# Kernel optimization log

Hardware: AMD Instinct MI355X
Metric: run time of the kernel (lower is better)

## Reference

```python
import jax, jax.numpy as jnp
import numpy as np

N_NODES = 50000
N_EDGES = 800000
IN_FT = 128
HID_FT = 64
EMB_FT = 128
NUM_LAYERS = 4
NEG_SLOP = 0.2


def setup_inputs() -> dict:
    key = jax.random.key(0)
    ks = jax.random.split(key, 16)
    x = jax.random.normal(ks[0], (N_NODES, IN_FT), dtype=jnp.float32)
    edge_index = jax.random.randint(ks[1], (2, N_EDGES), 0, N_NODES, dtype=jnp.int64)
    edge_weight = jax.random.uniform(ks[2], (N_EDGES,), dtype=jnp.float32)
    def lin(k, fin, fout):
        s = 1.0 / np.sqrt(fin)
        kw, kb = jax.random.split(k)
        W = jax.random.uniform(kw, (fin, fout), minval=-s, maxval=s, dtype=jnp.float32)
        b = jax.random.uniform(kb, (fout,), minval=-s, maxval=s, dtype=jnp.float32)
        return W, b
    W1, b1 = lin(ks[3], IN_FT, HID_FT)
    W2, b2 = lin(ks[4], HID_FT, HID_FT)
    W3, b3 = lin(ks[5], HID_FT, HID_FT)
    W4, b4 = lin(ks[6], HID_FT, HID_FT)
    Wh, bh = lin(ks[7], NUM_LAYERS * HID_FT, EMB_FT)
    return {"x": x, "edge_index": edge_index, "edge_weight": edge_weight,
            "W1": W1, "b1": b1, "W2": W2, "b2": b2, "W3": W3, "b3": b3,
            "W4": W4, "b4": b4, "Wh": Wh, "bh": bh}


def _gcn_no_norm(x, src, dst, ew, W, b):
    # GCNConv(add_self_loops=False, normalize=False): plain weighted scatter-add
    h = x @ W                                   # [N, F]
    msg = h[src] * ew[:, None]                  # gather over edges [E, F]
    return jax.ops.segment_sum(msg, dst, num_segments=N_NODES) + b


def _gcn_norm(x, src, dst, ew, W, b):
    # Default GCNConv: add self loops (weight 1) + symmetric normalization.
    deg = jax.ops.segment_sum(ew, dst, num_segments=N_NODES) + 1.0  # +1 self loop
    dinv = jnp.where(deg > 0, jax.lax.rsqrt(deg), 0.0)
    norm = dinv[src] * ew * dinv[dst]           # [E]
    h = x @ W
    agg = jax.ops.segment_sum(h[src] * norm[:, None], dst, num_segments=N_NODES)
    agg = agg + (dinv * dinv)[:, None] * h      # self-loop term
    return agg + b


def _forward(x, edge_index, edge_weight, W1, b1, W2, b2, W3, b3, W4, b4, Wh, bh):
    src, dst = edge_index[0], edge_index[1]
    lrelu = lambda v: jax.nn.leaky_relu(v, NEG_SLOP)
    outs = []
    h = lrelu(_gcn_no_norm(x, src, dst, edge_weight, W1, b1))
    outs.append(h)  # dropout is identity in deterministic reference
    for W, b in ((W2, b2), (W3, b3), (W4, b4)):
        h = lrelu(_gcn_norm(h, src, dst, edge_weight, W, b))
        outs.append(h)
    cat = jnp.concatenate(outs, axis=-1)        # [N, num_layers*HID_FT]
    return cat @ Wh + bh


def reference(x, edge_index, edge_weight, W1, b1, W2, b2, W3, b3, W4, b4, Wh, bh):
    return _forward(x, edge_index, edge_weight, W1, b1, W2, b2, W3, b3, W4, b4, Wh, bh)
```

## Files before the change

### kernel.cpp

```cpp
#include <hip/hip_runtime.h>
#include <hip/hip_bf16.h>

#define NEG_SLOP 0.2f
typedef unsigned long long ull;
typedef __attribute__((ext_vector_type(8))) short bf16x8;
typedef __attribute__((ext_vector_type(4))) float f32x4;

__device__ __forceinline__ float lrelu(float v) { return v > 0.0f ? v : NEG_SLOP * v; }

__device__ __forceinline__ float bf2f(unsigned short u) {
    union { unsigned int i; float f; } c; c.i = ((unsigned int)u) << 16; return c.f;
}
__device__ __forceinline__ unsigned short f2bf(float f) {
    union { float f; unsigned int i; } c; c.f = f;
    unsigned int r = c.i + 0x7FFF + ((c.i >> 16) & 1);
    return (unsigned short)(r >> 16);
}

__global__ void prep_kernel(const float* __restrict__ Wh, unsigned short* __restrict__ wht,
                            float4* __restrict__ pz, int nz) {
    int idx = blockIdx.x * 256 + threadIdx.x;
    if (idx < nz) pz[idx] = make_float4(0.f, 0.f, 0.f, 0.f);
    if (idx < 256 * 128) {
        int k = idx >> 7, c = idx & 127;
        wht[(size_t)c * 256 + k] = f2bf(Wh[idx]);
    }
}

__global__ void histo_kernel(const int* __restrict__ dst, const float* __restrict__ ew,
                             ull* __restrict__ packed4, int* __restrict__ rank,
                             int n_edges, int n) {
    int e = blockIdx.x * 256 + threadIdx.x;
    if (e >= n_edges) return;
    int d = dst[e];
    int c = e & 3;
    ull delta = (1ULL << 40) | (ull)(ew[e] * 4294967296.0f);
    ull old = atomicAdd(&packed4[(size_t)c * n + d], delta);
    rank[e] = (int)(old >> 40);
}

__global__ void dinv_kernel(const ull* __restrict__ packed4, float* __restrict__ dinv, int n) {
    int i = blockIdx.x * 256 + threadIdx.x;
    if (i >= n) return;
    const ull m = (1ULL << 40) - 1;
    ull s = (packed4[i] & m) + (packed4[(size_t)n + i] & m) +
            (packed4[2 * (size_t)n + i] & m) + (packed4[3 * (size_t)n + i] & m);
    float deg = (float)s * (1.0f / 4294967296.0f);
    dinv[i] = rsqrtf(deg + 1.0f);
}

__global__ void scan1_kernel(const ull* __restrict__ packed4, int* __restrict__ pre,
                             int4* __restrict__ bases, int* __restrict__ bsum, int n) {
    __shared__ int s[256];
    int t = threadIdx.x;
    int base = blockIdx.x * 1024 + t * 4;
    int tot[4];
#pragma unroll
    for (int j = 0; j < 4; ++j) {
        int node = base + j;
        if (node < n) {
            int c0 = (int)(packed4[node] >> 40);
            int c1 = (int)(packed4[(size_t)n + node] >> 40);
            int c2 = (int)(packed4[2 * (size_t)n + node] >> 40);
            int c3 = (int)(packed4[3 * (size_t)n + node] >> 40);
            bases[node] = make_int4(0, c0, c0 + c1, c0 + c1 + c2);
            tot[j] = c0 + c1 + c2 + c3;
        } else tot[j] = 0;
    }
    int tsum = tot[0] + tot[1] + tot[2] + tot[3];
    s[t] = tsum;
    __syncthreads();
    for (int off = 1; off < 256; off <<= 1) {
        int v = (t >= off) ? s[t - off] : 0;
        __syncthreads();
        s[t] += v;
        __syncthreads();
    }
    int ex = s[t] - tsum;
    if (t == 255) bsum[blockIdx.x] = s[255];
    int o[4];
    o[0] = ex; o[1] = ex + tot[0]; o[2] = o[1] + tot[1]; o[3] = o[2] + tot[2];
    if (base + 3 < n) *(int4*)&pre[base] = make_int4(o[0], o[1], o[2], o[3]);
    else {
        for (int j = 0; j < 4; ++j) if (base + j < n) pre[base + j] = o[j];
    }
}

__global__ void scan2_kernel(int* __restrict__ bsum, int nb) {
    __shared__ int s[64];
    int t = threadIdx.x;
    int v = (t < nb) ? bsum[t] : 0;
    s[t] = v;
    __syncthreads();
    for (int off = 1; off < 64; off <<= 1) {
        int u = (t >= off) ? s[t - off] : 0;
        __syncthreads();
        s[t] += u;
        __syncthreads();
    }
    if (t < nb) bsum[t] = s[t] - v;
}

__global__ void scan3_kernel(int* __restrict__ rp, const int* __restrict__ bsum,
                             int n, int n_edges) {
    int t = blockIdx.x * 256 + threadIdx.x;
    int base = t * 4;
    if (base >= n) {
        if (base == ((n + 3) & ~3)) rp[n] = n_edges;
        return;
    }
    int boff = bsum[base >> 10];
    if (base + 3 < n) {
        int4 v = *(const int4*)&rp[base];
        v.x += boff; v.y += boff; v.z += boff; v.w += boff;
        *(int4*)&rp[base] = v;
    } else {
        for (int j = 0; j < 4 && base + j < n; ++j) rp[base + j] += boff;
        rp[n] = n_edges;
    }
}

__global__ void fill_kernel(const int* __restrict__ src, const int* __restrict__ dst,
                            const float* __restrict__ ew, const int* __restrict__ rank,
                            const int* __restrict__ rp, const int4* __restrict__ bases,
                            int2* __restrict__ e_sw, int n_edges) {
    int e = blockIdx.x * 256 + threadIdx.x;
    if (e >= n_edges) return;
    int d = dst[e];
    int c = e & 3;
    int4 bs = bases[d];
    int b = (c == 0) ? bs.x : (c == 1) ? bs.y : (c == 2) ? bs.z : bs.w;
    int pos = rp[d] + b + rank[e];
    e_sw[pos] = make_int2(src[e], __float_as_int(ew[e]));
}

__global__ void gather_plain(const int* __restrict__ rp, const int2* __restrict__ e_sw,
                             const unsigned short* __restrict__ hb,
                             const float* __restrict__ b, unsigned short* __restrict__ cat, int n) {
    int node = (blockIdx.x * 256 + threadIdx.x) >> 6;
    if (node >= n) return;
    int lane = threadIdx.x & 63;
    int eg = lane >> 4;
    int f0 = (lane & 15) * 4;
    int lo = rp[node], hi = rp[node + 1];
    float a0 = 0.f, a1 = 0.f, a2 = 0.f, a3 = 0.f;
    for (int k = lo + eg; k < hi; k += 16) {
        int k1 = k + 4, k2 = k + 8, k3 = k + 12;
        int2 p0 = e_sw[k];
        int2 p1 = e_sw[k1 < hi ? k1 : k];
        int2 p2 = e_sw[k2 < hi ? k2 : k];
        int2 p3 = e_sw[k3 < hi ? k3 : k];
        float w0 = __int_as_float(p0.y);
        float w1 = k1 < hi ? __int_as_float(p1.y) : 0.f;
        float w2 = k2 < hi ? __int_as_float(p2.y) : 0.f;
        float w3 = k3 < hi ? __int_as_float(p3.y) : 0.f;
        ushort4 u0 = *(const ushort4*)&hb[(size_t)p0.x * 64 + f0];
        ushort4 u1 = *(const ushort4*)&hb[(size_t)p1.x * 64 + f0];
        ushort4 u2 = *(const ushort4*)&hb[(size_t)p2.x * 64 + f0];
        ushort4 u3 = *(const ushort4*)&hb[(size_t)p3.x * 64 + f0];
        a0 += w0 * bf2f(u0.x) + w1 * bf2f(u1.x) + w2 * bf2f(u2.x) + w3 * bf2f(u3.x);
        a1 += w0 * bf2f(u0.y) + w1 * bf2f(u1.y) + w2 * bf2f(u2.y) + w3 * bf2f(u3.y);
        a2 += w0 * bf2f(u0.z) + w1 * bf2f(u1.z) + w2 * bf2f(u2.z) + w3 * bf2f(u3.z);
        a3 += w0 * bf2f(u0.w) + w1 * bf2f(u1.w) + w2 * bf2f(u2.w) + w3 * bf2f(u3.w);
    }
    a0 += __shfl_xor(a0, 16, 64); a0 += __shfl_xor(a0, 32, 64);
    a1 += __shfl_xor(a1, 16, 64); a1 += __shfl_xor(a1, 32, 64);
    a2 += __shfl_xor(a2, 16, 64); a2 += __shfl_xor(a2, 32, 64);
    a3 += __shfl_xor(a3, 16, 64); a3 += __shfl_xor(a3, 32, 64);
    if (eg == 0) {
        ushort4 o;
        o.x = f2bf(lrelu(a0 + b[f0 + 0])); o.y = f2bf(lrelu(a1 + b[f0 + 1]));
        o.z = f2bf(lrelu(a2 + b[f0 + 2])); o.w = f2bf(lrelu(a3 + b[f0 + 3]));
        *(ushort4*)&cat[(size_t)node * 256 + f0] = o;
    }
}

__global__ void gather_norm(const int* __restrict__ rp, const int2* __restrict__ e_sw,
                            const unsigned short* __restrict__ hb,
                            const float* __restrict__ dinv, const float* __restrict__ b,
                            unsigned short* __restrict__ cat, int col_off, int n) {
    int node = (blockIdx.x * 256 + threadIdx.x) >> 6;
    if (node >= n) return;
    int lane = threadIdx.x & 63;
    int eg = lane >> 4;
    int f0 = (lane & 15) * 4;
    int lo = rp[node], hi = rp[node + 1];
    float a0 = 0.f, a1 = 0.f, a2 = 0.f, a3 = 0.f;
    for (int k = lo + eg; k < hi; k += 16) {
        int k1 = k + 4, k2 = k + 8, k3 = k + 12;
        int2 p0 = e_sw[k];
        int2 p1 = e_sw[k1 < hi ? k1 : k];
        int2 p2 = e_sw[k2 < hi ? k2 : k];
        int2 p3 = e_sw[k3 < hi ? k3 : k];
        float w0 = __int_as_float(p0.y);
        float w1 = k1 < hi ? __int_as_float(p1.y) : 0.f;
        float w2 = k2 < hi ? __int_as_float(p2.y) : 0.f;
        float w3 = k3 < hi ? __int_as_float(p3.y) : 0.f;
        ushort4 u0 = *(const ushort4*)&hb[(size_t)p0.x * 64 + f0];
        ushort4 u1 = *(const ushort4*)&hb[(size_t)p1.x * 64 + f0];
        ushort4 u2 = *(const ushort4*)&hb[(size_t)p2.x * 64 + f0];
        ushort4 u3 = *(const ushort4*)&hb[(size_t)p3.x * 64 + f0];
        a0 += w0 * bf2f(u0.x) + w1 * bf2f(u1.x) + w2 * bf2f(u2.x) + w3 * bf2f(u3.x);
        a1 += w0 * bf2f(u0.y) + w1 * bf2f(u1.y) + w2 * bf2f(u2.y) + w3 * bf2f(u3.y);
        a2 += w0 * bf2f(u0.z) + w1 * bf2f(u1.z) + w2 * bf2f(u2.z) + w3 * bf2f(u3.z);
        a3 += w0 * bf2f(u0.w) + w1 * bf2f(u1.w) + w2 * bf2f(u2.w) + w3 * bf2f(u3.w);
    }
    a0 += __shfl_xor(a0, 16, 64); a0 += __shfl_xor(a0, 32, 64);
    a1 += __shfl_xor(a1, 16, 64); a1 += __shfl_xor(a1, 32, 64);
    a2 += __shfl_xor(a2, 16, 64); a2 += __shfl_xor(a2, 32, 64);
    a3 += __shfl_xor(a3, 16, 64); a3 += __shfl_xor(a3, 32, 64);
    if (eg == 0) {
        float di = dinv[node];
        ushort4 h = *(const ushort4*)&hb[(size_t)node * 64 + f0];
        ushort4 o;
        o.x = f2bf(lrelu(di * (a0 + bf2f(h.x)) + b[f0 + 0]));
        o.y = f2bf(lrelu(di * (a1 + bf2f(h.y)) + b[f0 + 1]));
        o.z = f2bf(lrelu(di * (a2 + bf2f(h.z)) + b[f0 + 2]));
        o.w = f2bf(lrelu(di * (a3 + bf2f(h.w)) + b[f0 + 3]));
        *(ushort4*)&cat[(size_t)node * 256 + col_off + f0] = o;
    }
}

__global__ __launch_bounds__(256) void gemm_hid_f32(
    const float* __restrict__ in, int in_stride, int K,
    const float* __restrict__ W, unsigned short* __restrict__ outb, int n_rows) {
    __shared__ float Ws[64 * 64];
    __shared__ float XsT[64 * 132];
    const int tid = threadIdx.x;
    const int tc = tid & 15, tr = tid >> 4;
    const int row0 = blockIdx.x * 128;
    float acc[8][4] = {};
    for (int kc = 0; kc < K; kc += 64) {
        __syncthreads();
        for (int i = tid; i < 64 * 64; i += 256) Ws[i] = W[kc * 64 + i];
        {
            int k = tid & 63, rq = tid >> 6;
            for (int i = 0; i < 32; ++i) {
                int r = rq * 32 + i;
                int rr = row0 + r; if (rr >= n_rows) rr = n_rows - 1;
                XsT[k * 132 + r] = in[(size_t)rr * in_stride + kc + k];
            }
        }
        __syncthreads();
        for (int kk = 0; kk < 64; ++kk) {
            float4 w4 = *(const float4*)&Ws[kk * 64 + tc * 4];
            float4 aA = *(const float4*)&XsT[kk * 132 + tr * 8];
            float4 aB = *(const float4*)&XsT[kk * 132 + tr * 8 + 4];
            float a[8] = {aA.x, aA.y, aA.z, aA.w, aB.x, aB.y, aB.z, aB.w};
#pragma unroll
            for (int i = 0; i < 8; ++i) {
                acc[i][0] += a[i] * w4.x; acc[i][1] += a[i] * w4.y;
                acc[i][2] += a[i] * w4.z; acc[i][3] += a[i] * w4.w;
            }
        }
    }
#pragma unroll
    for (int i = 0; i < 8; ++i) {
        int r = row0 + tr * 8 + i;
        if (r >= n_rows) break;
        ushort4 o;
        o.x = f2bf(acc[i][0]); o.y = f2bf(acc[i][1]);
        o.z = f2bf(acc[i][2]); o.w = f2bf(acc[i][3]);
        *(ushort4*)&outb[(size_t)r * 64 + tc * 4] = o;
    }
}

__global__ __launch_bounds__(256) void gemm_hid_b(
    const unsigned short* __restrict__ in, int in_stride,
    const float* __restrict__ W, const float* __restrict__ dinv,
    unsigned short* __restrict__ outb, int n_rows) {
    __shared__ float Ws[64 * 64];
    __shared__ float XsT[64 * 132];
    const int tid = threadIdx.x;
    const int tc = tid & 15, tr = tid >> 4;
    const int row0 = blockIdx.x * 128;
    float acc[8][4] = {};
    for (int i = tid; i < 64 * 64; i += 256) Ws[i] = W[i];
    {
        int k2 = tid & 31, rq = tid >> 5;
        for (int i = 0; i < 16; ++i) {
            int r = rq * 16 + i;
            int rr = row0 + r; if (rr >= n_rows) rr = n_rows - 1;
            ushort2 u = *(const ushort2*)&in[(size_t)rr * in_stride + 2 * k2];
            XsT[(2 * k2) * 132 + r] = bf2f(u.x);
            XsT[(2 * k2 + 1) * 132 + r] = bf2f(u.y);
        }
    }
    __syncthreads();
    for (int kk = 0; kk < 64; ++kk) {
        float4 w4 = *(const float4*)&Ws[kk * 64 + tc * 4];
        float4 aA = *(const float4*)&XsT[kk * 132 + tr * 8];
        float4 aB = *(const float4*)&XsT[kk * 132 + tr * 8 + 4];
        float a[8] = {aA.x, aA.y, aA.z, aA.w, aB.x, aB.y, aB.z, aB.w};
#pragma unroll
        for (int i = 0; i < 8; ++i) {
            acc[i][0] += a[i] * w4.x; acc[i][1] += a[i] * w4.y;
            acc[i][2] += a[i] * w4.z; acc[i][3] += a[i] * w4.w;
        }
    }
#pragma unroll
    for (int i = 0; i < 8; ++i) {
        int r = row0 + tr * 8 + i;
        if (r >= n_rows) break;
        float di = dinv[r];
        ushort4 o;
        o.x = f2bf(acc[i][0] * di); o.y = f2bf(acc[i][1] * di);
        o.z = f2bf(acc[i][2] * di); o.w = f2bf(acc[i][3] * di);
        *(ushort4*)&outb[(size_t)r * 64 + tc * 4] = o;
    }
}

__global__ __launch_bounds__(256) void gemm_out_mfma(
    const unsigned short* __restrict__ cat, const unsigned short* __restrict__ whT,
    const float* __restrict__ bh, float* __restrict__ out, int n_rows) {
    __shared__ __align__(16) char As[64 * 128];
    __shared__ __align__(16) char Bs[128 * 128];
    const int tid = threadIdx.x;
    const int wid = tid >> 6, lane = tid & 63;
    const int row0 = blockIdx.x * 64;
    const int lrow = lane & 15, kg = lane >> 4;
    f32x4 acc[8] = {};
    for (int kc = 0; kc < 4; ++kc) {
        __syncthreads();
        {
            int row = tid >> 2, seg = tid & 3;
            int rr = row0 + row; if (rr >= n_rows) rr = n_rows - 1;
            const int4* g = (const int4*)&cat[(size_t)rr * 256 + kc * 64 + seg * 16];
            int4 u0 = g[0], u1 = g[1];
            int sw = (row & 7) << 4;
            int base = row * 128 + seg * 32;
            *(int4*)(As + (base ^ sw)) = u0;
            *(int4*)(As + ((base + 16) ^ sw)) = u1;
        }
        {
            int c = tid >> 1, seg = tid & 1;
            const int4* g = (const int4*)&whT[(size_t)c * 256 + kc * 64 + seg * 32];
            int sw = (c & 7) << 4;
            int base = c * 128 + seg * 64;
#pragma unroll
            for (int i = 0; i < 4; ++i)
                *(int4*)(Bs + ((base + i * 16) ^ sw)) = g[i];
        }
        __syncthreads();
        int arow = wid * 16 + lrow;
        int asw = (arow & 7) << 4;
#pragma unroll
        for (int ks = 0; ks < 2; ++ks) {
            bf16x8 af = *(bf16x8*)(As + ((arow * 128 + ks * 64 + kg * 16) ^ asw));
#pragma unroll
            for (int cf = 0; cf < 8; ++cf) {
                int c = cf * 16 + lrow;
                bf16x8 bf = *(bf16x8*)(Bs + ((c * 128 + ks * 64 + kg * 16) ^ ((c & 7) << 4)));
                acc[cf] = __builtin_amdgcn_mfma_f32_16x16x32_bf16(af, bf, acc[cf], 0, 0, 0);
            }
        }
    }
    int lrow4 = (lane >> 4) * 4;
#pragma unroll
    for (int cf = 0; cf < 8; ++cf) {
        int col = cf * 16 + lrow;
        float bias = bh[col];
#pragma unroll
        for (int reg = 0; reg < 4; ++reg) {
            int r = row0 + wid * 16 + lrow4 + reg;
            if (r < n_rows) out[(size_t)r * 128 + col] = acc[cf][reg] + bias;
        }
    }
}

extern "C" void kernel_launch(void* const* d_in, const int* in_sizes, int n_in,
                              void* d_out, int out_size, void* d_ws, size_t ws_size,
                              hipStream_t stream) {
    const float* x  = (const float*)d_in[0];
    const int*   ei = (const int*)d_in[1];
    const float* ew = (const float*)d_in[2];
    const float* W1 = (const float*)d_in[3];
    const float* b1 = (const float*)d_in[4];
    const float* W2 = (const float*)d_in[5];
    const float* b2 = (const float*)d_in[6];
    const float* W3 = (const float*)d_in[7];
    const float* b3 = (const float*)d_in[8];
    const float* W4 = (const float*)d_in[9];
    const float* b4 = (const float*)d_in[10];
    const float* Wh = (const float*)d_in[11];
    const float* bh = (const float*)d_in[12];

    const int E = in_sizes[2];
    const int N = in_sizes[0] / 128;
    const int* src = ei;
    const int* dst = ei + E;

    char* p = (char*)d_ws;
    unsigned short* cat     = (unsigned short*)p; p += (size_t)N * 256 * 2;
    unsigned short* hb      = (unsigned short*)p; p += (size_t)N * 64 * 2;
    unsigned short* wht     = (unsigned short*)p; p += (size_t)128 * 256 * 2;
    ull*            packed4 = (ull*)p;            p += (size_t)N * 4 * 8;
    float*          dinv    = (float*)p;          p += (size_t)N * 4;
    int*            row_ptr = (int*)p;            p += (size_t)(N + 4) * 4;
    int*            bsum    = (int*)p;            p += (size_t)64 * 4;
    int4*           bases   = (int4*)p;           p += (size_t)N * 16;
    int*            rank    = (int*)p;            p += (size_t)E * 4;
    int2*           e_sw    = (int2*)p;           p += (size_t)E * 8;
    float* out = (float*)d_out;

    int eb   = (E + 255) / 256;
    int nb   = (N + 255) / 256;
    int nb64 = (N * 64 + 255) / 256;
    int gb   = (N + 127) / 128;
    int gb64 = (N + 63) / 64;
    int sb   = (N + 1023) / 1024;
    int s3b  = ((N + 3) / 4 + 256) / 256;
    int nz   = N * 2;
    int pb   = (nz > 256 * 128 ? nz : 256 * 128) / 256 + 1;

    prep_kernel<<<pb, 256, 0, stream>>>(Wh, wht, (float4*)packed4, nz);
    histo_kernel<<<eb, 256, 0, stream>>>(dst, ew, packed4, rank, E, N);
    dinv_kernel<<<nb, 256, 0, stream>>>(packed4, dinv, N);
    scan1_kernel<<<sb, 256, 0, stream>>>(packed4, row_ptr, bases, bsum, N);
    scan2_kernel<<<1, 64, 0, stream>>>(bsum, sb);
    scan3_kernel<<<s3b, 256, 0, stream>>>(row_ptr, bsum, N, E);
    fill_kernel<<<eb, 256, 0, stream>>>(src, dst, ew, rank, row_ptr, bases, e_sw, E);

    gemm_hid_f32<<<gb, 256, 0, stream>>>(x, 128, 128, W1, hb, N);
    gather_plain<<<nb64, 256, 0, stream>>>(row_ptr, e_sw, hb, b1, cat, N);

    const float* Wl[3] = {W2, W3, W4};
    const float* bl[3] = {b2, b3, b4};
    for (int l = 1; l < 4; ++l) {
        gemm_hid_b<<<gb, 256, 0, stream>>>(cat + (size_t)(l - 1) * 64, 256, Wl[l - 1],
                                           dinv, hb, N);
        gather_norm<<<nb64, 256, 0, stream>>>(row_ptr, e_sw, hb, dinv,
                                              bl[l - 1], cat, l * 64, N);
    }

    gemm_out_mfma<<<gb64, 256, 0, stream>>>(cat, wht, bh, out, N);
}
```

Before: 259.7 us.

## Move hidden-layer GEMMs to bf16 MFMA and fold dinv into scan

Replaces the scalar fp32 FMA hidden-layer GEMMs (first layer from x, later layers from bf16 cat) with bf16 MFMA 16x16x32 kernels that use swizzled LDS tiles and pre-transposed bf16 weights, which prep_kernel now produces. The separate dinv kernel is removed and its degree computation is merged into scan1, which already reads packed4, saving one launch and one pass over packed4. The first layer now rounds x to bf16 before the matmul, which lowers input precision compared with the fp32 path. The output stores are scalar 2-byte writes, so they may coalesce less well than before.

```diff
diff --git a/kernel.cpp b/kernel.cpp
--- a/kernel.cpp
+++ b/kernel.cpp
@@ -18,12 +18,26 @@
 }
 
 __global__ void prep_kernel(const float* __restrict__ Wh, unsigned short* __restrict__ wht,
+                            const float* __restrict__ W1, unsigned short* __restrict__ w1t,
+                            const float* __restrict__ W2, unsigned short* __restrict__ w2t,
+                            const float* __restrict__ W3, unsigned short* __restrict__ w3t,
+                            const float* __restrict__ W4, unsigned short* __restrict__ w4t,
                             float4* __restrict__ pz, int nz) {
     int idx = blockIdx.x * 256 + threadIdx.x;
     if (idx < nz) pz[idx] = make_float4(0.f, 0.f, 0.f, 0.f);
     if (idx < 256 * 128) {
         int k = idx >> 7, c = idx & 127;
         wht[(size_t)c * 256 + k] = f2bf(Wh[idx]);
+    }
+    if (idx < 64 * 128) {
+        int c = idx >> 7, k = idx & 127;
+        w1t[idx] = f2bf(W1[k * 64 + c]);
+    }
+    if (idx < 64 * 64) {
+        int c = idx >> 6, k = idx & 63;
+        w2t[idx] = f2bf(W2[k * 64 + c]);
+        w3t[idx] = f2bf(W3[k * 64 + c]);
+        w4t[idx] = f2bf(W4[k * 64 + c]);
     }
 }
 
@@ -39,32 +53,29 @@
     rank[e] = (int)(old >> 40);
 }
 
-__global__ void dinv_kernel(const ull* __restrict__ packed4, float* __restrict__ dinv, int n) {
-    int i = blockIdx.x * 256 + threadIdx.x;
-    if (i >= n) return;
-    const ull m = (1ULL << 40) - 1;
-    ull s = (packed4[i] & m) + (packed4[(size_t)n + i] & m) +
-            (packed4[2 * (size_t)n + i] & m) + (packed4[3 * (size_t)n + i] & m);
-    float deg = (float)s * (1.0f / 4294967296.0f);
-    dinv[i] = rsqrtf(deg + 1.0f);
-}
-
 __global__ void scan1_kernel(const ull* __restrict__ packed4, int* __restrict__ pre,
-                             int4* __restrict__ bases, int* __restrict__ bsum, int n) {
+                             int4* __restrict__ bases, int* __restrict__ bsum,
+                             float* __restrict__ dinv, int n) {
     __shared__ int s[256];
     int t = threadIdx.x;
     int base = blockIdx.x * 1024 + t * 4;
+    const ull m = (1ULL << 40) - 1;
     int tot[4];
 #pragma unroll
     for (int j = 0; j < 4; ++j) {
         int node = base + j;
         if (node < n) {
-            int c0 = (int)(packed4[node] >> 40);
-            int c1 = (int)(packed4[(size_t)n + node] >> 40);
-            int c2 = (int)(packed4[2 * (size_t)n + node] >> 40);
-            int c3 = (int)(packed4[3 * (size_t)n + node] >> 40);
+            ull p0 = packed4[node];
+            ull p1 = packed4[(size_t)n + node];
+            ull p2 = packed4[2 * (size_t)n + node];
+            ull p3 = packed4[3 * (size_t)n + node];
+            int c0 = (int)(p0 >> 40), c1 = (int)(p1 >> 40);
+            int c2 = (int)(p2 >> 40), c3 = (int)(p3 >> 40);
             bases[node] = make_int4(0, c0, c0 + c1, c0 + c1 + c2);
             tot[j] = c0 + c1 + c2 + c3;
+            float deg = (float)((p0 & m) + (p1 & m) + (p2 & m) + (p3 & m)) *
+                        (1.0f / 4294967296.0f);
+            dinv[node] = rsqrtf(deg + 1.0f);
         } else tot[j] = 0;
     }
     int tsum = tot[0] + tot[1] + tot[2] + tot[3];
@@ -221,92 +232,104 @@
     }
 }
 
-__global__ __launch_bounds__(256) void gemm_hid_f32(
-    const float* __restrict__ in, int in_stride, int K,
-    const float* __restrict__ W, unsigned short* __restrict__ outb, int n_rows) {
-    __shared__ float Ws[64 * 64];
-    __shared__ float XsT[64 * 132];
+__global__ __launch_bounds__(256) void gemm_hid_mfma(
+    const unsigned short* __restrict__ in, int in_stride,
+    const unsigned short* __restrict__ wT,
+    const float* __restrict__ dinv,
+    unsigned short* __restrict__ outb, int n_rows) {
+    __shared__ __align__(16) char As[64 * 128];
+    __shared__ __align__(16) char Bs[64 * 128];
     const int tid = threadIdx.x;
-    const int tc = tid & 15, tr = tid >> 4;
-    const int row0 = blockIdx.x * 128;
-    float acc[8][4] = {};
-    for (int kc = 0; kc < K; kc += 64) {
-        __syncthreads();
-        for (int i = tid; i < 64 * 64; i += 256) Ws[i] = W[kc * 64 + i];
-        {
-            int k = tid & 63, rq = tid >> 6;
-            for (int i = 0; i < 32; ++i) {
-                int r = rq * 32 + i;
-                int rr = row0 + r; if (rr >= n_rows) rr = n_rows - 1;
-                XsT[k * 132 + r] = in[(size_t)rr * in_stride + kc + k];
-            }
-        }
-        __syncthreads();
-        for (int kk = 0; kk < 64; ++kk) {
-            float4 w4 = *(const float4*)&Ws[kk * 64 + tc * 4];
-            float4 aA = *(const float4*)&XsT[kk * 132 + tr * 8];
-            float4 aB = *(const float4*)&XsT[kk * 132 + tr * 8 + 4];
-            float a[8] = {aA.x, aA.y, aA.z, aA.w, aB.x, aB.y, aB.z, aB.w};
-#pragma unroll
-            for (int i = 0; i < 8; ++i) {
-                acc[i][0] += a[i] * w4.x; acc[i][1] += a[i] * w4.y;
-                acc[i][2] += a[i] * w4.z; acc[i][3] += a[i] * w4.w;
-            }
-        }
-    }
-#pragma unroll
-    for (int i = 0; i < 8; ++i) {
-        int r = row0 + tr * 8 + i;
-        if (r >= n_rows) break;
-        ushort4 o;
-        o.x = f2bf(acc[i][0]); o.y = f2bf(acc[i][1]);
-        o.z = f2bf(acc[i][2]); o.w = f2bf(acc[i][3]);
-        *(ushort4*)&outb[(size_t)r * 64 + tc * 4] = o;
-    }
-}
-
-__global__ __launch_bounds__(256) void gemm_hid_b(
-    const unsigned short* __restrict__ in, int in_stride,
-    const float* __restrict__ W, const float* __restrict__ dinv,
+    const int wid = tid >> 6, lane = tid & 63;
+    const int row0 = blockIdx.x * 64;
+    const int lrow = lane & 15, kg = lane >> 4;
+    {
+        int row = tid >> 2, seg = tid & 3;
+        int rr = row0 + row; if (rr >= n_rows) rr = n_rows - 1;
+        const int4* g = (const int4*)&in[(size_t)rr * in_stride + seg * 16];
+        int4 u0 = g[0], u1 = g[1];
+        const int4* gb = (const int4*)&wT[(size_t)row * 64 + seg * 16];
+        int4 v0 = gb[0], v1 = gb[1];
+        int sw = (row & 7) << 4;
+        int base = row * 128 + seg * 32;
+        *(int4*)(As + (base ^ sw)) = u0;
+        *(int4*)(As + ((base + 16) ^ sw)) = u1;
+        *(int4*)(Bs + (base ^ sw)) = v0;
+        *(int4*)(Bs + ((base + 16) ^ sw)) = v1;
+    }
+    __syncthreads();
+    int arow = wid * 16 + lrow;
+    int asw = (arow & 7) << 4;
+    f32x4 acc[4] = {};
+#pragma unroll
+    for (int ks = 0; ks < 2; ++ks) {
+        bf16x8 af = *(bf16x8*)(As + ((arow * 128 + ks * 64 + kg * 16) ^ asw));
+#pragma unroll
+        for (int cf = 0; cf < 4; ++cf) {
+            int c = cf * 16 + lrow;
+            bf16x8 bf = *(bf16x8*)(Bs + ((c * 128 + ks * 64 + kg * 16) ^ ((c & 7) << 4)));
+            acc[cf] = __builtin_amdgcn_mfma_f32_16x16x32_bf16(af, bf, acc[cf], 0, 0, 0);
+        }
+    }
+    int r4 = (lane >> 4) * 4;
+#pragma unroll
+    for (int reg = 0; reg < 4; ++reg) {
+        int r = row0 + wid * 16 + r4 + reg;
+        if (r >= n_rows) continue;
+        float di = dinv[r];
+#pragma unroll
+        for (int cf = 0; cf < 4; ++cf)
+            outb[(size_t)r * 64 + cf * 16 + lrow] = f2bf(acc[cf][reg] * di);
+    }
+}
+
+__global__ __launch_bounds__(256) void gemm_hid_mfma_x(
+    const float* __restrict__ x, const unsigned short* __restrict__ w1T,
     unsigned short* __restrict__ outb, int n_rows) {
-    __shared__ float Ws[64 * 64];
-    __shared__ float XsT[64 * 132];
+    __shared__ __align__(16) char As[64 * 256];
+    __shared__ __align__(16) char Bs[64 * 256];
     const int tid = threadIdx.x;
-    const int tc = tid & 15, tr = tid >> 4;
-    const int row0 = blockIdx.x * 128;
-    float acc[8][4] = {};
-    for (int i = tid; i < 64 * 64; i += 256) Ws[i] = W[i];
+    const int wid = tid >> 6, lane = tid & 63;
+    const int row0 = blockIdx.x * 64;
+    const int lrow = lane & 15, kg = lane >> 4;
     {
-        int k2 = tid & 31, rq = tid >> 5;
-        for (int i = 0; i < 16; ++i) {
-            int r = rq * 16 + i;
-            int rr = row0 + r; if (rr >= n_rows) rr = n_rows - 1;
-            ushort2 u = *(const ushort2*)&in[(size_t)rr * in_stride + 2 * k2];
-            XsT[(2 * k2) * 132 + r] = bf2f(u.x);
-            XsT[(2 * k2 + 1) * 132 + r] = bf2f(u.y);
+        int row = tid >> 2, seg = tid & 3;
+        int rr = row0 + row; if (rr >= n_rows) rr = n_rows - 1;
+        const float4* g = (const float4*)&x[(size_t)rr * 128 + seg * 32];
+        const int4* gb = (const int4*)&w1T[(size_t)row * 128 + seg * 32];
+        int sw = (row & 7) << 4;
+        int base = row * 256 + seg * 64;
+#pragma unroll
+        for (int i = 0; i < 4; ++i) {
+            float4 f0 = g[2 * i], f1 = g[2 * i + 1];
+            unsigned short u[8] = {f2bf(f0.x), f2bf(f0.y), f2bf(f0.z), f2bf(f0.w),
+                                   f2bf(f1.x), f2bf(f1.y), f2bf(f1.z), f2bf(f1.w)};
+            *(int4*)(As + ((base + i * 16) ^ sw)) = *(int4*)u;
+            *(int4*)(Bs + ((base + i * 16) ^ sw)) = gb[i];
         }
     }
     __syncthreads();
-    for (int kk = 0; kk < 64; ++kk) {
-        float4 w4 = *(const float4*)&Ws[kk * 64 + tc * 4];
-        float4 aA = *(const float4*)&XsT[kk * 132 + tr * 8];
-        float4 aB = *(const float4*)&XsT[kk * 132 + tr * 8 + 4];
-        float a[8] = {aA.x, aA.y, aA.z, aA.w, aB.x, aB.y, aB.z, aB.w};
-#pragma unroll
-        for (int i = 0; i < 8; ++i) {
-            acc[i][0] += a[i] * w4.x; acc[i][1] += a[i] * w4.y;
-            acc[i][2] += a[i] * w4.z; acc[i][3] += a[i] * w4.w;
-        }
-    }
-#pragma unroll
-    for (int i = 0; i < 8; ++i) {
-        int r = row0 + tr * 8 + i;
-        if (r >= n_rows) break;
-        float di = dinv[r];
-        ushort4 o;
-        o.x = f2bf(acc[i][0] * di); o.y = f2bf(acc[i][1] * di);
-        o.z = f2bf(acc[i][2] * di); o.w = f2bf(acc[i][3] * di);
-        *(ushort4*)&outb[(size_t)r * 64 + tc * 4] = o;
+    int arow = wid * 16 + lrow;
+    int asw = (arow & 7) << 4;
+    f32x4 acc[4] = {};
+#pragma unroll
+    for (int ks = 0; ks < 4; ++ks) {
+        bf16x8 af = *(bf16x8*)(As + ((arow * 256 + ks * 64 + kg * 16) ^ asw));
+#pragma unroll
+        for (int cf = 0; cf < 4; ++cf) {
+            int c = cf * 16 + lrow;
+            bf16x8 bf = *(bf16x8*)(Bs + ((c * 256 + ks * 64 + kg * 16) ^ ((c & 7) << 4)));
+            acc[cf] = __builtin_amdgcn_mfma_f32_16x16x32_bf16(af, bf, acc[cf], 0, 0, 0);
+        }
+    }
+    int r4 = (lane >> 4) * 4;
+#pragma unroll
+    for (int reg = 0; reg < 4; ++reg) {
+        int r = row0 + wid * 16 + r4 + reg;
+        if (r >= n_rows) continue;
+#pragma unroll
+        for (int cf = 0; cf < 4; ++cf)
+            outb[(size_t)r * 64 + cf * 16 + lrow] = f2bf(acc[cf][reg]);
     }
 }
 
@@ -394,6 +417,10 @@
     unsigned short* cat     = (unsigned short*)p; p += (size_t)N * 256 * 2;
     unsigned short* hb      = (unsigned short*)p; p += (size_t)N * 64 * 2;
     unsigned short* wht     = (unsigned short*)p; p += (size_t)128 * 256 * 2;
+    unsigned short* w1t     = (unsigned short*)p; p += (size_t)64 * 128 * 2;
+    unsigned short* w2t     = (unsigned short*)p; p += (size_t)64 * 64 * 2;
+    unsigned short* w3t     = (unsigned short*)p; p += (size_t)64 * 64 * 2;
+    unsigned short* w4t     = (unsigned short*)p; p += (size_t)64 * 64 * 2;
     ull*            packed4 = (ull*)p;            p += (size_t)N * 4 * 8;
     float*          dinv    = (float*)p;          p += (size_t)N * 4;
     int*            row_ptr = (int*)p;            p += (size_t)(N + 4) * 4;
@@ -404,31 +431,29 @@
     float* out = (float*)d_out;
 
     int eb   = (E + 255) / 256;
-    int nb   = (N + 255) / 256;
     int nb64 = (N * 64 + 255) / 256;
-    int gb   = (N + 127) / 128;
     int gb64 = (N + 63) / 64;
     int sb   = (N + 1023) / 1024;
     int s3b  = ((N + 3) / 4 + 256) / 256;
     int nz   = N * 2;
     int pb   = (nz > 256 * 128 ? nz : 256 * 128) / 256 + 1;
 
-    prep_kernel<<<pb, 256, 0, stream>>>(Wh, wht, (float4*)packed4, nz);
+    prep_kernel<<<pb, 256, 0, stream>>>(Wh, wht, W1, w1t, W2, w2t, W3, w3t, W4, w4t,
+                                        (float4*)packed4, nz);
     histo_kernel<<<eb, 256, 0, stream>>>(dst, ew, packed4, rank, E, N);
-    dinv_kernel<<<nb, 256, 0, stream>>>(packed4, dinv, N);
-    scan1_kernel<<<sb, 256, 0, stream>>>(packed4, row_ptr, bases, bsum, N);
+    scan1_kernel<<<sb, 256, 0, stream>>>(packed4, row_ptr, bases, bsum, dinv, N);
     scan2_kernel<<<1, 64, 0, stream>>>(bsum, sb);
     scan3_kernel<<<s3b, 256, 0, stream>>>(row_ptr, bsum, N, E);
     fill_kernel<<<eb, 256, 0, stream>>>(src, dst, ew, rank, row_ptr, bases, e_sw, E);
 
-    gemm_hid_f32<<<gb, 256, 0, stream>>>(x, 128, 128, W1, hb, N);
+    gemm_hid_mfma_x<<<gb64, 256, 0, stream>>>(x, w1t, hb, N);
     gather_plain<<<nb64, 256, 0, stream>>>(row_ptr, e_sw, hb, b1, cat, N);
 
-    const float* Wl[3] = {W2, W3, W4};
+    const unsigned short* Wt[3] = {w2t, w3t, w4t};
     const float* bl[3] = {b2, b3, b4};
     for (int l = 1; l < 4; ++l) {
-        gemm_hid_b<<<gb, 256, 0, stream>>>(cat + (size_t)(l - 1) * 64, 256, Wl[l - 1],
-                                           dinv, hb, N);
+        gemm_hid_mfma<<<gb64, 256, 0, stream>>>(cat + (size_t)(l - 1) * 64, 256,
+                                                Wt[l - 1], dinv, hb, N);
         gather_norm<<<nb64, 256, 0, stream>>>(row_ptr, e_sw, hb, dinv,
                                               bl[l - 1], cat, l * 64, N);
     }
```

Result: faster. 219.0 us (-15.7%).
